# Performance work log

Measured on AMD Instinct MI355X. Metric: run time of the kernel, lower is better.

## Reference

```python
import jax, jax.numpy as jnp
import numpy as np

DIM = 1024
HEADS = 16
HEAD_DIM = DIM // HEADS
SCALE = HEAD_DIM ** -0.5


def setup_inputs() -> dict:
    key = jax.random.key(0)
    k_x, k_wqkv, k_bqkv, k_wp, k_bp = jax.random.split(key, 5)
    B, N, C = 8, 1024, DIM
    lim_qkv = 1.0 / np.sqrt(C)
    x = jax.random.normal(k_x, (B, N, C), dtype=jnp.float32)
    # store weights in [in, out] layout (torch Linear weight is [out,in]; y = x @ W.T + b)
    W_qkv = jax.random.uniform(k_wqkv, (C, 3 * C), dtype=jnp.float32, minval=-lim_qkv, maxval=lim_qkv)
    b_qkv = jax.random.uniform(k_bqkv, (3 * C,), dtype=jnp.float32, minval=-lim_qkv, maxval=lim_qkv)
    W_proj = jax.random.uniform(k_wp, (C, C), dtype=jnp.float32, minval=-lim_qkv, maxval=lim_qkv)
    b_proj = jax.random.uniform(k_bp, (C,), dtype=jnp.float32, minval=-lim_qkv, maxval=lim_qkv)
    return {"x": x, "W_qkv": W_qkv, "b_qkv": b_qkv, "W_proj": W_proj, "b_proj": b_proj}


def reference(x, W_qkv, b_qkv, W_proj, b_proj):
    B, N, C = x.shape
    H, D = HEADS, C // HEADS
    qkv = x @ W_qkv + b_qkv                          # [B, N, 3C]
    qkv = qkv.reshape(B, N, 3, H, D)
    q, k, v = jnp.moveaxis(qkv, 2, 0)                # each [B, N, H, D]
    q = q.transpose(0, 2, 1, 3)                      # [B, H, N, D]
    k = k.transpose(0, 2, 1, 3)
    v = v.transpose(0, 2, 1, 3)
    attn = jnp.einsum("bhnd,bhmd->bhnm", q, k) * SCALE
    attn = jax.nn.softmax(attn, axis=-1)
    out = jnp.einsum("bhnm,bhmd->bhnd", attn, v)     # [B, H, N, D]
    out = out.transpose(0, 2, 1, 3).reshape(B, N, C)
    return out @ W_proj + b_proj
```

## Files before the change

kernel.cpp:

```cpp
#include <hip/hip_runtime.h>
#include <hip/hip_bf16.h>


using bf16x8 = __attribute__((ext_vector_type(8))) short;
using f32x4  = __attribute__((ext_vector_type(4))) float;
using u16    = unsigned short;
using u16x8  = __attribute__((ext_vector_type(8))) unsigned short;
using u32x2  = __attribute__((ext_vector_type(2))) unsigned int;

__device__ __forceinline__ u16 f2bf(float f) {
  unsigned int u = __float_as_uint(f);
  u += 0x7FFFu + ((u >> 16) & 1u);
  return (u16)(u >> 16);
}
__device__ __forceinline__ float bf2f(u16 h) {
  return __uint_as_float(((unsigned int)h) << 16);
}
__device__ __forceinline__ unsigned cvt_pk_bf16(float a, float b) {
  unsigned r;
  asm("v_cvt_pk_bf16_f32 %0, %1, %2" : "=v"(r) : "v"(a), "v"(b));
  return r;
}
__device__ __forceinline__ float fexp2(float x) {
#if __has_builtin(__builtin_amdgcn_exp2f)
  return __builtin_amdgcn_exp2f(x);
#else
  return exp2f(x);
#endif
}

__device__ __forceinline__ void gload16(const u16* g, u16* lbase, int lane) {
#if __has_builtin(__builtin_amdgcn_global_load_lds)
  __builtin_amdgcn_global_load_lds(
      (const __attribute__((address_space(1))) void*)g,
      (__attribute__((address_space(3))) void*)lbase, 16, 0, 0);
#else
  *(u16x8*)(lbase + (size_t)lane * 8) = *(const u16x8*)g;
#endif
}

__device__ __forceinline__ void transpose_tile(
    const float* __restrict__ W, u16* __restrict__ Wt, int K, int N,
    int n0, int k0, float (*T)[65], int t)
{
  const int r = t >> 4, c4 = (t & 15) * 4;
  #pragma unroll
  for (int i = 0; i < 4; ++i) {
    f32x4 v = *(const f32x4*)&W[(size_t)(k0 + r + i * 16) * N + n0 + c4];
    T[r + i * 16][c4 + 0] = v.x;
    T[r + i * 16][c4 + 1] = v.y;
    T[r + i * 16][c4 + 2] = v.z;
    T[r + i * 16][c4 + 3] = v.w;
  }
  __syncthreads();
  const int nr = t >> 2, cs = (t & 3) * 16;
  u16x8 h0, h1;
  #pragma unroll
  for (int j = 0; j < 8; ++j) h0[j] = f2bf(T[cs + j][nr]);
  #pragma unroll
  for (int j = 0; j < 8; ++j) h1[j] = f2bf(T[cs + 8 + j][nr]);
  u16* dst = Wt + (size_t)(n0 + nr) * K + k0 + cs;
  *(u16x8*)dst = h0;
  *(u16x8*)(dst + 8) = h1;
}

__global__ __launch_bounds__(256) void prep(
    const float* __restrict__ x, u16* __restrict__ Xb,
    const float* __restrict__ Wq, u16* __restrict__ Wqt,
    const float* __restrict__ Wp, u16* __restrict__ Wpt)
{
  __shared__ float T[64][65];
  const int bid = blockIdx.x, t = threadIdx.x;
  if (bid < 4096) {
    size_t i = ((size_t)bid * 256 + t) * 8;
    f32x4 a = *(const f32x4*)(x + i);
    f32x4 b = *(const f32x4*)(x + i + 4);
    u16x8 h = { f2bf(a.x), f2bf(a.y), f2bf(a.z), f2bf(a.w),
                f2bf(b.x), f2bf(b.y), f2bf(b.z), f2bf(b.w) };
    *(u16x8*)(Xb + i) = h;
  } else if (bid < 4864) {
    const int tb = bid - 4096;
    transpose_tile(Wq, Wqt, 1024, 3072, (tb % 48) * 64, (tb / 48) * 64, T, t);
  } else {
    const int tb = bid - 4864;
    transpose_tile(Wp, Wpt, 1024, 1024, (tb % 16) * 64, (tb / 16) * 64, T, t);
  }
}

__global__ __launch_bounds__(256, 2) void qkv_gemm2(
    const u16* __restrict__ Xb, const u16* __restrict__ Wt,
    const float* __restrict__ bias,
    u16* __restrict__ Qb, u16* __restrict__ Kb, u16* __restrict__ VtG)
{
  constexpr int KD = 1024;
  __shared__ __align__(16) u16 SM[128 * 130];
  u16* As = SM;
  u16* Bs = SM + 4096;
  u16* Tv = SM;

  const int tid = threadIdx.x;
  const int lane = tid & 63, wid = tid >> 6;
  const int wr = wid >> 1, wc = wid & 1;
  const int lg = lane >> 4, lc = lane & 15;
  const int row0 = blockIdx.x * 128, col0 = blockIdx.y * 128;

  f32x4 acc[4][4];
  #pragma unroll
  for (int m = 0; m < 4; ++m)
    #pragma unroll
    for (int n = 0; n < 4; ++n) acc[m][n] = (f32x4){0.f, 0.f, 0.f, 0.f};

  const int l4 = lane >> 2, ls = (lane & 3) * 8;
  const u16* gA0 = Xb + (size_t)(row0 + wid * 16 + l4) * KD + ls;
  const u16* gB0 = Wt + (size_t)(col0 + wid * 16 + l4) * KD + ls;
  u16* lA0 = As + wid * 512;
  u16* lB0 = Bs + wid * 512;

  for (int k0 = 0; k0 < KD; k0 += 32) {
    gload16(gA0 + k0, lA0, lane);
    gload16(gA0 + 64 * KD + k0, lA0 + 2048, lane);
    gload16(gB0 + k0, lB0, lane);
    gload16(gB0 + 64 * KD + k0, lB0 + 2048, lane);
    __syncthreads();

    bf16x8 a[4], b[4];
    #pragma unroll
    for (int m = 0; m < 4; ++m)
      a[m] = *(const bf16x8*)(As + (wr * 64 + m * 16 + lc) * 32 + lg * 8);
    #pragma unroll
    for (int n = 0; n < 4; ++n)
      b[n] = *(const bf16x8*)(Bs + (wc * 64 + n * 16 + lc) * 32 + lg * 8);
    #pragma unroll
    for (int m = 0; m < 4; ++m)
      #pragma unroll
      for (int n = 0; n < 4; ++n)
        acc[m][n] = __builtin_amdgcn_mfma_f32_16x16x32_bf16(a[m], b[n], acc[m][n], 0, 0, 0);
    __syncthreads();
  }

  const int which = col0 >> 10;
  if (which == 2) {
    #pragma unroll
    for (int m = 0; m < 4; ++m) {
      #pragma unroll
      for (int n = 0; n < 4; ++n) {
        const int col = wc * 64 + n * 16 + lc;
        const float bv = bias[col0 + col];
        const int rrow = wr * 64 + m * 16 + lg * 4;
        #pragma unroll
        for (int r = 0; r < 4; ++r)
          Tv[(rrow + r) * 130 + col] = f2bf(acc[m][n][r] + bv);
      }
    }
    __syncthreads();
    const int c = tid >> 1, half = tid & 1;
    const int hh = c >> 6, d = c & 63;
    const int bb = row0 >> 10, nb = row0 & 1023;
    const int hbase = (col0 & 1023) >> 6;
    u16* vdst = VtG + ((size_t)(bb * 16 + hbase + hh) * 64 + d) * 1024
                + nb + half * 64;
    #pragma unroll
    for (int g = 0; g < 8; ++g) {
      u16x8 o;
      #pragma unroll
      for (int j = 0; j < 8; ++j)
        o[j] = Tv[(half * 64 + g * 8 + j) * 130 + c];
      *(u16x8*)(vdst + g * 8) = o;
    }
  } else {
    u16* dst = (which == 0) ? Qb : Kb;
    #pragma unroll
    for (int m = 0; m < 4; ++m) {
      #pragma unroll
      for (int n = 0; n < 4; ++n) {
        const int gc = col0 + wc * 64 + n * 16 + lc;
        const float bv = bias[gc];
        const int ci = gc & 1023, h = ci >> 6, d = ci & 63;
        const int gr0 = row0 + wr * 64 + m * 16 + lg * 4;
        const int bb = gr0 >> 10, nn0 = gr0 & 1023;
        #pragma unroll
        for (int r = 0; r < 4; ++r)
          dst[((size_t)(bb * 16 + h) * 1024 + nn0 + r) * 64 + d] =
              f2bf(acc[m][n][r] + bv);
      }
    }
  }
}

__global__ __launch_bounds__(256, 2) void attn_kernel(
    const u16* __restrict__ Q, const u16* __restrict__ K,
    const u16* __restrict__ Vt, u16* __restrict__ O)
{
  __shared__ __align__(16) u16 Ks[64 * 64];
  __shared__ __align__(16) u16 Vs[64 * 64];
  __shared__ __align__(16) u16 Pl[4 * 32 * 72];

  const int tid = threadIdx.x, lane = tid & 63, wid = tid >> 6;
  const int lg = lane >> 4, lc = lane & 15;
  const int bh = blockIdx.x;
  const int qt = blockIdx.y;
  const size_t base = (size_t)bh * 65536;
  const u16* Qp = Q + base;
  const u16* Kp = K + base;
  const u16* Vp = Vt + base;

  const float QSCALE = 0.125f * 1.44269504f;
  bf16x8 qf[2][2];
  #pragma unroll
  for (int f = 0; f < 2; ++f) {
    const u16* qsrc = Qp + (size_t)(qt * 128 + wid * 32 + f * 16 + lc) * 64 + lg * 8;
    #pragma unroll
    for (int ks = 0; ks < 2; ++ks) {
      u16x8 raw = *(const u16x8*)(qsrc + ks * 32);
      bf16x8 t;
      #pragma unroll
      for (int j = 0; j < 8; ++j) t[j] = (short)f2bf(bf2f(raw[j]) * QSCALE);
      qf[f][ks] = t;
    }
  }

  f32x4 o[2][4];
  #pragma unroll
  for (int f = 0; f < 2; ++f)
    #pragma unroll
    for (int d = 0; d < 4; ++d) o[f][d] = (f32x4){0.f, 0.f, 0.f, 0.f};
  float m_r[2] = {-1e30f, -1e30f};
  float l_r[2] = {0.f, 0.f};

  const int srow  = lane >> 3;
  const int sslot = (lane & 7) ^ srow;
  const u16* gK0 = Kp + (size_t)(wid * 16 + srow) * 64 + sslot * 8;
  const u16* gV0 = Vp + (size_t)(wid * 16 + srow) * 1024 + sslot * 8;
  u16* lK0 = Ks + wid * 1024;
  u16* lV0 = Vs + wid * 1024;

  const int xr = lc & 7;
  const int cof0 = ((0 + lg) ^ xr) * 8;
  const int cof1 = ((4 + lg) ^ xr) * 8;
  const int prow = (wid * 32 + lc) * 72;

  for (int kt = 0; kt < 16; ++kt) {
    gload16(gK0 + kt * 4096, lK0, lane);
    gload16(gK0 + kt * 4096 + 512, lK0 + 512, lane);
    gload16(gV0 + kt * 64, lV0, lane);
    gload16(gV0 + 8192 + kt * 64, lV0 + 512, lane);
    __syncthreads();

    f32x4 s[2][4];
    #pragma unroll
    for (int f = 0; f < 2; ++f)
      #pragma unroll
      for (int kb = 0; kb < 4; ++kb) s[f][kb] = (f32x4){0.f, 0.f, 0.f, 0.f};
    #pragma unroll
    for (int ks = 0; ks < 2; ++ks) {
      const int co = ks ? cof1 : cof0;
      #pragma unroll
      for (int kb = 0; kb < 4; ++kb) {
        bf16x8 kfr = *(const bf16x8*)(Ks + (kb * 16 + lc) * 64 + co);
        s[0][kb] = __builtin_amdgcn_mfma_f32_16x16x32_bf16(kfr, qf[0][ks], s[0][kb], 0, 0, 0);
        s[1][kb] = __builtin_amdgcn_mfma_f32_16x16x32_bf16(kfr, qf[1][ks], s[1][kb], 0, 0, 0);
      }
    }

    #pragma unroll
    for (int f = 0; f < 2; ++f) {
      f32x4 t01, t23;
      #pragma unroll
      for (int c = 0; c < 4; ++c) {
        t01[c] = fmaxf(s[f][0][c], s[f][1][c]);
        t23[c] = fmaxf(s[f][2][c], s[f][3][c]);
      }
      float t = fmaxf(fmaxf(fmaxf(t01[0], t01[1]), fmaxf(t01[2], t01[3])),
                      fmaxf(fmaxf(t23[0], t23[1]), fmaxf(t23[2], t23[3])));
      t = fmaxf(t, __shfl_xor(t, 16));
      t = fmaxf(t, __shfl_xor(t, 32));

      if (!__all((t - m_r[f]) <= 11.5f)) {
        float nm = fmaxf(m_r[f], t);
        float sc = fexp2(m_r[f] - nm);
        m_r[f] = nm;
        l_r[f] *= sc;
        #pragma unroll
        for (int r = 0; r < 4; ++r) {
          float scr = __shfl(sc, lg * 4 + r, 16);
          #pragma unroll
          for (int d = 0; d < 4; ++d) o[f][d][r] *= scr;
        }
      }

      float lsum = 0.f;
      #pragma unroll
      for (int kb = 0; kb < 4; ++kb) {
        f32x4 p;
        #pragma unroll
        for (int c = 0; c < 4; ++c) {
          p[c] = fexp2(s[f][kb][c] - m_r[f]);
          lsum += p[c];
        }
        u32x2 w = { cvt_pk_bf16(p[0], p[1]), cvt_pk_bf16(p[2], p[3]) };
        *(u32x2*)(Pl + prow + f * 1152 + kb * 16 + lg * 4) = w;
      }
      l_r[f] += lsum;
    }

    bf16x8 pa[2][2];
    #pragma unroll
    for (int f = 0; f < 2; ++f)
      #pragma unroll
      for (int ks = 0; ks < 2; ++ks)
        pa[f][ks] = *(const bf16x8*)(Pl + prow + f * 1152 + ks * 32 + lg * 8);
    #pragma unroll
    for (int d = 0; d < 4; ++d) {
      #pragma unroll
      for (int ks = 0; ks < 2; ++ks) {
        const int co = ks ? cof1 : cof0;
        bf16x8 vfr = *(const bf16x8*)(Vs + (d * 16 + lc) * 64 + co);
        o[0][d] = __builtin_amdgcn_mfma_f32_16x16x32_bf16(pa[0][ks], vfr, o[0][d], 0, 0, 0);
        o[1][d] = __builtin_amdgcn_mfma_f32_16x16x32_bf16(pa[1][ks], vfr, o[1][d], 0, 0, 0);
      }
    }
    __syncthreads();
  }

  const int b = bh >> 4, h = bh & 15;
  #pragma unroll
  for (int f = 0; f < 2; ++f) {
    float t = l_r[f];
    t += __shfl_xor(t, 16);
    t += __shfl_xor(t, 32);
    float linv = 1.0f / t;
    #pragma unroll
    for (int r = 0; r < 4; ++r) {
      float li = __shfl(linv, lg * 4 + r, 16);
      int n = qt * 128 + wid * 32 + f * 16 + lg * 4 + r;
      u16* dst = O + ((size_t)b * 1024 + n) * 1024 + h * 64 + lc;
      #pragma unroll
      for (int d = 0; d < 4; ++d) dst[d * 16] = f2bf(o[f][d][r] * li);
    }
  }
}

__global__ __launch_bounds__(256, 2) void proj_gemm2(
    const u16* __restrict__ Ab, const u16* __restrict__ Wt,
    const float* __restrict__ bias, float* __restrict__ Out)
{
  constexpr int KD = 1024, NCOL = 1024;
  __shared__ __align__(16) u16 As[128 * 32];
  __shared__ __align__(16) u16 Bs[128 * 32];

  const int tid = threadIdx.x;
  const int lane = tid & 63, wid = tid >> 6;
  const int wr = wid >> 1, wc = wid & 1;
  const int lg = lane >> 4, lc = lane & 15;
  const int row0 = blockIdx.x * 128, col0 = blockIdx.y * 128;

  f32x4 acc[4][4];
  #pragma unroll
  for (int m = 0; m < 4; ++m)
    #pragma unroll
    for (int n = 0; n < 4; ++n) acc[m][n] = (f32x4){0.f, 0.f, 0.f, 0.f};

  const int l4 = lane >> 2, ls = (lane & 3) * 8;
  const u16* gA0 = Ab + (size_t)(row0 + wid * 16 + l4) * KD + ls;
  const u16* gB0 = Wt + (size_t)(col0 + wid * 16 + l4) * KD + ls;
  u16* lA0 = As + wid * 512;
  u16* lB0 = Bs + wid * 512;

  for (int k0 = 0; k0 < KD; k0 += 32) {
    gload16(gA0 + k0, lA0, lane);
    gload16(gA0 + 64 * KD + k0, lA0 + 2048, lane);
    gload16(gB0 + k0, lB0, lane);
    gload16(gB0 + 64 * KD + k0, lB0 + 2048, lane);
    __syncthreads();

    bf16x8 a[4], b[4];
    #pragma unroll
    for (int m = 0; m < 4; ++m)
      a[m] = *(const bf16x8*)(As + (wr * 64 + m * 16 + lc) * 32 + lg * 8);
    #pragma unroll
    for (int n = 0; n < 4; ++n)
      b[n] = *(const bf16x8*)(Bs + (wc * 64 + n * 16 + lc) * 32 + lg * 8);
    #pragma unroll
    for (int m = 0; m < 4; ++m)
      #pragma unroll
      for (int n = 0; n < 4; ++n)
        acc[m][n] = __builtin_amdgcn_mfma_f32_16x16x32_bf16(a[m], b[n], acc[m][n], 0, 0, 0);
    __syncthreads();
  }

  #pragma unroll
  for (int m = 0; m < 4; ++m) {
    #pragma unroll
    for (int n = 0; n < 4; ++n) {
      #pragma unroll
      for (int r = 0; r < 4; ++r) {
        int gr = row0 + wr * 64 + m * 16 + lg * 4 + r;
        int gc = col0 + wc * 64 + n * 16 + lc;
        Out[(size_t)gr * NCOL + gc] = acc[m][n][r] + bias[gc];
      }
    }
  }
}

extern "C" void kernel_launch(void* const* d_in, const int* in_sizes, int n_in,
                              void* d_out, int out_size, void* d_ws, size_t ws_size,
                              hipStream_t stream) {
  const float* x     = (const float*)d_in[0];
  const float* W_qkv = (const float*)d_in[1];
  const float* b_qkv = (const float*)d_in[2];
  const float* W_prj = (const float*)d_in[3];
  const float* b_prj = (const float*)d_in[4];
  float* out = (float*)d_out;

  const size_t SEG = (size_t)8192 * 1024;
  char* ws = (char*)d_ws;
  u16* Xb  = (u16*)ws;
  u16* Ab  = Xb;
  u16* VtG = (u16*)(ws + SEG * 2);
  u16* Wqt = (u16*)(ws + SEG * 4);
  u16* Wpt = Wqt + (size_t)3072 * 1024;
  u16* Qb  = (u16*)d_out;
  u16* Kb  = Qb + SEG;

  prep<<<5120, 256, 0, stream>>>(x, Xb, W_qkv, Wqt, W_prj, Wpt);
  qkv_gemm2<<<dim3(64, 24), 256, 0, stream>>>(Xb, Wqt, b_qkv, Qb, Kb, VtG);
  attn_kernel<<<dim3(128, 8), 256, 0, stream>>>(Qb, Kb, VtG, Ab);
  proj_gemm2<<<dim3(64, 8), 256, 0, stream>>>(Ab, Wpt, b_prj, out);
}
```

Baseline: 159.7 us.

## Double GEMM K-tile to 64 with XOR-swizzled LDS and MFMA priority hints

Both the QKV and projection GEMMs now stage K-tiles of 64 instead of 32 through a shared macro. This halves the number of barrier pairs per output tile, and an XOR swizzle on the LDS slot layout is meant to avoid bank conflicts on the fragment reads. s_setprio hints are also wrapped around the MFMA bursts in the GEMMs and the attention kernel to favour matrix issue. In exchange, the projection kernel uses twice as much LDS, and any swizzle mismatch between the write side and the read side would corrupt results.

```diff
diff --git a/kernel.cpp b/kernel.cpp
--- a/kernel.cpp
+++ b/kernel.cpp
@@ -87,56 +87,68 @@
   }
 }
 
+#define GEMM64_LOOP(ABASE, BBASE, AS, BS)                                     \
+  const int tid = threadIdx.x;                                                \
+  const int lane = tid & 63, wid = tid >> 6;                                  \
+  const int wr = wid >> 1, wc = wid & 1;                                      \
+  const int lg = lane >> 4, lc = lane & 15;                                   \
+  const int row0 = blockIdx.x * 128, col0 = blockIdx.y * 128;                 \
+  f32x4 acc[4][4];                                                            \
+  _Pragma("unroll")                                                           \
+  for (int m = 0; m < 4; ++m)                                                 \
+    _Pragma("unroll")                                                         \
+    for (int n = 0; n < 4; ++n) acc[m][n] = (f32x4){0.f, 0.f, 0.f, 0.f};      \
+             \
+  const int srow = lane >> 3;                                       \
+  const int sslot = (lane & 7) ^ srow;             \
+  const u16* gA = (ABASE) + (size_t)(row0 + wid * 32 + srow) * 1024 + sslot * 8; \
+  const u16* gB = (BBASE) + (size_t)(col0 + wid * 32 + srow) * 1024 + sslot * 8; \
+  u16* lA = (AS) + wid * 2048;                                                \
+  u16* lB = (BS) + wid * 2048;                                                \
+       \
+  const int xr = lc & 7;                                                      \
+  const int sl0 = ((0 + lg) ^ xr) * 8, sl1 = ((4 + lg) ^ xr) * 8;             \
+  const int arow = (wr * 64 + lc) * 64, brow = (wc * 64 + lc) * 64;           \
+  for (int k0 = 0; k0 < 1024; k0 += 64) {                                     \
+    _Pragma("unroll")                                                         \
+    for (int c = 0; c < 4; ++c) {                                             \
+      gload16(gA + (size_t)c * 8192 + k0, lA + c * 512, lane);                \
+      gload16(gB + (size_t)c * 8192 + k0, lB + c * 512, lane);                \
+    }                                                                         \
+    __syncthreads();                                                          \
+    _Pragma("unroll")                                                         \
+    for (int ks = 0; ks < 2; ++ks) {                                          \
+      const int sl = ks ? sl1 : sl0;                                          \
+      bf16x8 a[4], b[4];                                                      \
+      _Pragma("unroll")                                                       \
+      for (int m = 0; m < 4; ++m)                                             \
+        a[m] = *(const bf16x8*)((AS) + arow + m * 1024 + sl);                 \
+      _Pragma("unroll")                                                       \
+      for (int n = 0; n < 4; ++n)                                             \
+        b[n] = *(const bf16x8*)((BS) + brow + n * 1024 + sl);                 \
+      __builtin_amdgcn_s_setprio(1);                                          \
+      _Pragma("unroll")                                                       \
+      for (int m = 0; m < 4; ++m)                                             \
+        _Pragma("unroll")                                                     \
+        for (int n = 0; n < 4; ++n)                                           \
+          acc[m][n] = __builtin_amdgcn_mfma_f32_16x16x32_bf16(                \
+              a[m], b[n], acc[m][n], 0, 0, 0);                                \
+      __builtin_amdgcn_s_setprio(0);                                          \
+    }                                                                         \
+    __syncthreads();                                                          \
+  }
+
 __global__ __launch_bounds__(256, 2) void qkv_gemm2(
     const u16* __restrict__ Xb, const u16* __restrict__ Wt,
     const float* __restrict__ bias,
     u16* __restrict__ Qb, u16* __restrict__ Kb, u16* __restrict__ VtG)
 {
-  constexpr int KD = 1024;
   __shared__ __align__(16) u16 SM[128 * 130];
   u16* As = SM;
-  u16* Bs = SM + 4096;
+  u16* Bs = SM + 8192;
   u16* Tv = SM;
 
-  const int tid = threadIdx.x;
-  const int lane = tid & 63, wid = tid >> 6;
-  const int wr = wid >> 1, wc = wid & 1;
-  const int lg = lane >> 4, lc = lane & 15;
-  const int row0 = blockIdx.x * 128, col0 = blockIdx.y * 128;
-
-  f32x4 acc[4][4];
-  #pragma unroll
-  for (int m = 0; m < 4; ++m)
-    #pragma unroll
-    for (int n = 0; n < 4; ++n) acc[m][n] = (f32x4){0.f, 0.f, 0.f, 0.f};
-
-  const int l4 = lane >> 2, ls = (lane & 3) * 8;
-  const u16* gA0 = Xb + (size_t)(row0 + wid * 16 + l4) * KD + ls;
-  const u16* gB0 = Wt + (size_t)(col0 + wid * 16 + l4) * KD + ls;
-  u16* lA0 = As + wid * 512;
-  u16* lB0 = Bs + wid * 512;
-
-  for (int k0 = 0; k0 < KD; k0 += 32) {
-    gload16(gA0 + k0, lA0, lane);
-    gload16(gA0 + 64 * KD + k0, lA0 + 2048, lane);
-    gload16(gB0 + k0, lB0, lane);
-    gload16(gB0 + 64 * KD + k0, lB0 + 2048, lane);
-    __syncthreads();
-
-    bf16x8 a[4], b[4];
-    #pragma unroll
-    for (int m = 0; m < 4; ++m)
-      a[m] = *(const bf16x8*)(As + (wr * 64 + m * 16 + lc) * 32 + lg * 8);
-    #pragma unroll
-    for (int n = 0; n < 4; ++n)
-      b[n] = *(const bf16x8*)(Bs + (wc * 64 + n * 16 + lc) * 32 + lg * 8);
-    #pragma unroll
-    for (int m = 0; m < 4; ++m)
-      #pragma unroll
-      for (int n = 0; n < 4; ++n)
-        acc[m][n] = __builtin_amdgcn_mfma_f32_16x16x32_bf16(a[m], b[n], acc[m][n], 0, 0, 0);
-    __syncthreads();
-  }
+  GEMM64_LOOP(Xb, Wt, As, Bs)
 
   const int which = col0 >> 10;
   if (which == 2) {
@@ -251,6 +263,7 @@
     for (int f = 0; f < 2; ++f)
       #pragma unroll
       for (int kb = 0; kb < 4; ++kb) s[f][kb] = (f32x4){0.f, 0.f, 0.f, 0.f};
+    __builtin_amdgcn_s_setprio(1);
     #pragma unroll
     for (int ks = 0; ks < 2; ++ks) {
       const int co = ks ? cof1 : cof0;
@@ -261,6 +274,7 @@
         s[1][kb] = __builtin_amdgcn_mfma_f32_16x16x32_bf16(kfr, qf[1][ks], s[1][kb], 0, 0, 0);
       }
     }
+    __builtin_amdgcn_s_setprio(0);
 
     #pragma unroll
     for (int f = 0; f < 2; ++f) {
@@ -309,6 +323,7 @@
       #pragma unroll
       for (int ks = 0; ks < 2; ++ks)
         pa[f][ks] = *(const bf16x8*)(Pl + prow + f * 1152 + ks * 32 + lg * 8);
+    __builtin_amdgcn_s_setprio(1);
     #pragma unroll
     for (int d = 0; d < 4; ++d) {
       #pragma unroll
@@ -319,6 +334,7 @@
         o[1][d] = __builtin_amdgcn_mfma_f32_16x16x32_bf16(pa[1][ks], vfr, o[1][d], 0, 0, 0);
       }
     }
+    __builtin_amdgcn_s_setprio(0);
     __syncthreads();
   }
 
@@ -344,49 +360,10 @@
     const u16* __restrict__ Ab, const u16* __restrict__ Wt,
     const float* __restrict__ bias, float* __restrict__ Out)
 {
-  constexpr int KD = 1024, NCOL = 1024;
-  __shared__ __align__(16) u16 As[128 * 32];
-  __shared__ __align__(16) u16 Bs[128 * 32];
-
-  const int tid = threadIdx.x;
-  const int lane = tid & 63, wid = tid >> 6;
-  const int wr = wid >> 1, wc = wid & 1;
-  const int lg = lane >> 4, lc = lane & 15;
-  const int row0 = blockIdx.x * 128, col0 = blockIdx.y * 128;
-
-  f32x4 acc[4][4];
-  #pragma unroll
-  for (int m = 0; m < 4; ++m)
-    #pragma unroll
-    for (int n = 0; n < 4; ++n) acc[m][n] = (f32x4){0.f, 0.f, 0.f, 0.f};
-
-  const int l4 = lane >> 2, ls = (lane & 3) * 8;
-  const u16* gA0 = Ab + (size_t)(row0 + wid * 16 + l4) * KD + ls;
-  const u16* gB0 = Wt + (size_t)(col0 + wid * 16 + l4) * KD + ls;
-  u16* lA0 = As + wid * 512;
-  u16* lB0 = Bs + wid * 512;
-
-  for (int k0 = 0; k0 < KD; k0 += 32) {
-    gload16(gA0 + k0, lA0, lane);
-    gload16(gA0 + 64 * KD + k0, lA0 + 2048, lane);
-    gload16(gB0 + k0, lB0, lane);
-    gload16(gB0 + 64 * KD + k0, lB0 + 2048, lane);
-    __syncthreads();
-
-    bf16x8 a[4], b[4];
-    #pragma unroll
-    for (int m = 0; m < 4; ++m)
-      a[m] = *(const bf16x8*)(As + (wr * 64 + m * 16 + lc) * 32 + lg * 8);
-    #pragma unroll
-    for (int n = 0; n < 4; ++n)
-      b[n] = *(const bf16x8*)(Bs + (wc * 64 + n * 16 + lc) * 32 + lg * 8);
-    #pragma unroll
-    for (int m = 0; m < 4; ++m)
-      #pragma unroll
-      for (int n = 0; n < 4; ++n)
-        acc[m][n] = __builtin_amdgcn_mfma_f32_16x16x32_bf16(a[m], b[n], acc[m][n], 0, 0, 0);
-    __syncthreads();
-  }
+  __shared__ __align__(16) u16 As[128 * 64];
+  __shared__ __align__(16) u16 Bs[128 * 64];
+
+  GEMM64_LOOP(Ab, Wt, As, Bs)
 
   #pragma unroll
   for (int m = 0; m < 4; ++m) {
@@ -396,7 +373,7 @@
       for (int r = 0; r < 4; ++r) {
         int gr = row0 + wr * 64 + m * 16 + lg * 4 + r;
         int gc = col0 + wc * 64 + n * 16 + lc;
-        Out[(size_t)gr * NCOL + gc] = acc[m][n][r] + bias[gc];
+        Out[(size_t)gr * 1024 + gc] = acc[m][n][r] + bias[gc];
       }
     }
   }
```

Result: no change. 158.7 us (-0.6%).
